# Optimization experiments

Hardware: AMD Instinct MI355X
Metric: run time of the kernel (lower is better)

## Reference

```python
import jax, jax.numpy as jnp
from jax import lax
import numpy as np

T, B, NIN, H, NOUT = 256, 64, 512, 512, 512


def _lstm_dir(x, w_ih, w_hh, b_ih, b_hh, reverse):
    # x: [T,B,NIN]; w_ih: [4H,NIN]; w_hh: [4H,H]
    xg = jnp.einsum('tbi,gi->tbg', x, w_ih) + b_ih + b_hh  # [T,B,4H]
    if reverse:
        xg = xg[::-1]
    h0 = jnp.zeros((x.shape[1], w_hh.shape[1]), x.dtype)

    def step(carry, g):
        h, c = carry
        g = g + h @ w_hh.T
        i, f, gg, o = jnp.split(g, 4, axis=-1)  # PyTorch gate order i,f,g,o
        i = jax.nn.sigmoid(i)
        f = jax.nn.sigmoid(f)
        gg = jnp.tanh(gg)
        o = jax.nn.sigmoid(o)
        c = f * c + i * gg
        h = o * jnp.tanh(c)
        return (h, c), h

    _, hs = lax.scan(step, (h0, h0), xg)
    if reverse:
        hs = hs[::-1]
    return hs  # [T,B,H]


def setup_inputs() -> dict:
    key = jax.random.key(0)
    ks = jax.random.split(key, 12)
    s_in = 1.0 / np.sqrt(H)
    u = lambda k, shape: jax.random.uniform(k, shape, jnp.float32, -s_in, s_in)
    return {
        'x': jax.random.normal(ks[0], (T, B, NIN), jnp.float32),
        'w_ih_f': u(ks[1], (4 * H, NIN)),
        'w_hh_f': u(ks[2], (4 * H, H)),
        'b_ih_f': u(ks[3], (4 * H,)),
        'b_hh_f': u(ks[4], (4 * H,)),
        'w_ih_b': u(ks[5], (4 * H, NIN)),
        'w_hh_b': u(ks[6], (4 * H, H)),
        'b_ih_b': u(ks[7], (4 * H,)),
        'b_hh_b': u(ks[8], (4 * H,)),
        'fc_w': u(ks[9], (NOUT, 2 * H)),
        'fc_b': u(ks[10], (NOUT,)),
    }


def reference(x, w_ih_f, w_hh_f, b_ih_f, b_hh_f, w_ih_b, w_hh_b, b_ih_b, b_hh_b, fc_w, fc_b):
    h_f = _lstm_dir(x, w_ih_f, w_hh_f, b_ih_f, b_hh_f, reverse=False)
    h_b = _lstm_dir(x, w_ih_b, w_hh_b, b_ih_b, b_hh_b, reverse=True)
    h = jnp.concatenate([h_f, h_b], axis=-1)  # [T,B,2H]
    out = jnp.einsum('tbh,oh->tbo', h, fc_w) + fc_b  # fused linear over T*B rows
    return out
```

## Files before the change

kernel.cpp:

```cpp
#include <hip/hip_runtime.h>

typedef unsigned short u16;
typedef unsigned int u32;
typedef unsigned long long u64;
typedef short v8s __attribute__((ext_vector_type(8)));
typedef float v4f __attribute__((ext_vector_type(4)));

#define TT 256
#define BB 64
#define HH 512
#define G4 2048
#define MTB 16384

static __device__ __forceinline__ float bf2f(u16 u) {
    u32 x = ((u32)u) << 16;
    union { u32 i; float f; } c; c.i = x; return c.f;
}
static __device__ __forceinline__ u16 f2bf(float f) {
    union { float f; u32 i; } c; c.f = f;
    u32 u = c.i;
    u += 0x7fffu + ((u >> 16) & 1u);
    return (u16)(u >> 16);
}

__global__ __launch_bounds__(256) void cvt_bf16(const float* __restrict__ src,
                                                u16* __restrict__ dst, int n) {
    int i = blockIdx.x * blockDim.x + threadIdx.x;
    int stride = gridDim.x * blockDim.x;
    for (int j = i * 4; j < n; j += stride * 4) {
        float4 v = *reinterpret_cast<const float4*>(src + j);
        ushort4 o;
        o.x = f2bf(v.x); o.y = f2bf(v.y); o.z = f2bf(v.z); o.w = f2bf(v.w);
        *reinterpret_cast<ushort4*>(dst + j) = o;
    }
}

template<bool OUT_BF16, bool BIAS_M>
__global__ __launch_bounds__(256) void gemm_bt(const u16* __restrict__ A,
                                               const u16* __restrict__ Bm,
                                               void* __restrict__ Cv,
                                               const float* __restrict__ bias1,
                                               const float* __restrict__ bias2,
                                               int M, int N, int K) {
    __shared__ u16 lds_a[128 * 64];
    __shared__ u16 lds_b[128 * 64];
    const int tid = threadIdx.x, lane = tid & 63;
    const int m0 = blockIdx.y * 128, n0 = blockIdx.x * 128;
    const int wid = tid >> 6, wm = wid >> 1, wn = wid & 1;
    v4f acc[4][4] = {};

    const int srow  = tid >> 3;
    const int skoff = (tid & 7) * 8;
    const u16* Ag = A + (size_t)(m0 + srow) * K + skoff;
    const u16* Bg = Bm + (size_t)(n0 + srow) * K + skoff;
    u16* la = lds_a + srow * 64 + skoff;
    u16* lb = lds_b + srow * 64 + skoff;

    for (int k0 = 0; k0 < K; k0 += 64) {
        #pragma unroll
        for (int q = 0; q < 4; ++q) {
            *reinterpret_cast<v8s*>(la + q * 32 * 64) =
                *reinterpret_cast<const v8s*>(Ag + (size_t)q * 32 * K + k0);
            *reinterpret_cast<v8s*>(lb + q * 32 * 64) =
                *reinterpret_cast<const v8s*>(Bg + (size_t)q * 32 * K + k0);
        }
        __syncthreads();
        #pragma unroll
        for (int kk = 0; kk < 2; ++kk) {
            v8s af[4], bfr[4];
            #pragma unroll
            for (int i = 0; i < 4; ++i)
                af[i] = *reinterpret_cast<const v8s*>(
                    lds_a + (wm * 64 + i * 16 + (lane & 15)) * 64 + kk * 32 + (lane >> 4) * 8);
            #pragma unroll
            for (int i = 0; i < 4; ++i)
                bfr[i] = *reinterpret_cast<const v8s*>(
                    lds_b + (wn * 64 + i * 16 + (lane & 15)) * 64 + kk * 32 + (lane >> 4) * 8);
            #pragma unroll
            for (int i = 0; i < 4; ++i)
                #pragma unroll
                for (int j = 0; j < 4; ++j)
                    acc[i][j] = __builtin_amdgcn_mfma_f32_16x16x32_bf16(af[i], bfr[j], acc[i][j], 0, 0, 0);
        }
        __syncthreads();
    }
    #pragma unroll
    for (int i = 0; i < 4; ++i) {
        #pragma unroll
        for (int j = 0; j < 4; ++j) {
            #pragma unroll
            for (int r = 0; r < 4; ++r) {
                int m = m0 + wm * 64 + i * 16 + (lane >> 4) * 4 + r;
                int n = n0 + wn * 64 + j * 16 + (lane & 15);
                float v = acc[i][j][r];
                if (BIAS_M) { v += bias1[m]; if (bias2) v += bias2[m]; }
                else        { v += bias1[n]; }
                if (OUT_BF16) ((u16*)Cv)[(size_t)m * N + n] = f2bf(v);
                else          ((float*)Cv)[(size_t)m * N + n] = v;
            }
        }
    }
}

static __device__ __forceinline__ float sigm(float x) { return 1.f / (1.f + __expf(-x)); }
static __device__ __forceinline__ float tanh_(float x) { return 2.f / (1.f + __expf(-2.f * x)) - 1.f; }

__global__ __launch_bounds__(256, 2) void lstm_persist(
    const u16* __restrict__ w_hh,
    const u16* __restrict__ xgT,
    u16* __restrict__ h_all,
    unsigned* __restrict__ flags)
{
    __shared__ u16 wlds[4 * 16 * 64 * 8];
    const int bx = blockIdx.x;
    const int d = bx >> 5, cg = bx & 31;
    const int lane = threadIdx.x & 63, nf = threadIdx.x >> 6;
    const int lrow = lane & 15, lk = lane >> 4;
    const int b = nf * 16 + lrow;

    {
        const int G = nf;
        const u16* wrow = w_hh + ((size_t)d * G4 + G * HH + cg * 16 + lrow) * HH + lk * 8;
        #pragma unroll
        for (int kk = 0; kk < 16; ++kk)
            *reinterpret_cast<v8s*>(&wlds[((G * 16 + kk) * 64 + lane) * 8]) =
                *reinterpret_cast<const v8s*>(wrow + kk * 32);
    }
    __syncthreads();

    float c[4] = {0.f, 0.f, 0.f, 0.f};
    float xg[4][4];
    unsigned* cnt = flags + (d * 4 + nf) * 64;

    {
        const int t0 = d ? (TT - 1) : 0;
        const u16* xgb = xgT + (size_t)d * G4 * MTB + (size_t)t0 * BB + b;
        #pragma unroll
        for (int G = 0; G < 4; ++G)
            #pragma unroll
            for (int r = 0; r < 4; ++r)
                xg[G][r] = bf2f(xgb[(size_t)(G * HH + cg * 16 + lk * 4 + r) * MTB]);
    }

    for (int s = 0; s < TT; ++s) {
        const int t = d ? (TT - 1 - s) : s;
        v4f acc[4] = {};
        if (s > 0) {
            v8s af0[4][4];
            #pragma unroll
            for (int G = 0; G < 4; ++G)
                #pragma unroll
                for (int kk = 0; kk < 4; ++kk)
                    af0[G][kk] = *reinterpret_cast<const v8s*>(
                        &wlds[((G * 16 + kk) * 64 + lane) * 8]);
            const unsigned tgt = 32u * (unsigned)s;
            while (true) {
                unsigned fv = __hip_atomic_load(cnt, __ATOMIC_RELAXED,
                                                __HIP_MEMORY_SCOPE_AGENT);
                if (__all((int)(fv >= tgt))) break;
            }
            asm volatile("" ::: "memory");
            const int tprev = d ? (t + 1) : (t - 1);
            const u16* hp = h_all + ((size_t)tprev * BB + b) * 1024 + d * HH + lk * 8;
            v8s bf_[16];
            #pragma unroll
            for (int kk = 0; kk < 16; ++kk) {
                union { u64 w[2]; v8s v; } u;
                const u16* p = hp + kk * 32;
                u.w[0] = __hip_atomic_load((const u64*)p,
                                           __ATOMIC_RELAXED, __HIP_MEMORY_SCOPE_AGENT);
                u.w[1] = __hip_atomic_load((const u64*)(p + 4),
                                           __ATOMIC_RELAXED, __HIP_MEMORY_SCOPE_AGENT);
                bf_[kk] = u.v;
            }
            #pragma unroll
            for (int kk = 0; kk < 4; ++kk)
                #pragma unroll
                for (int G = 0; G < 4; ++G)
                    acc[G] = __builtin_amdgcn_mfma_f32_16x16x32_bf16(af0[G][kk], bf_[kk], acc[G], 0, 0, 0);
            #pragma unroll
            for (int kk = 4; kk < 16; ++kk)
                #pragma unroll
                for (int G = 0; G < 4; ++G) {
                    v8s af = *reinterpret_cast<const v8s*>(
                        &wlds[((G * 16 + kk) * 64 + lane) * 8]);
                    acc[G] = __builtin_amdgcn_mfma_f32_16x16x32_bf16(af, bf_[kk], acc[G], 0, 0, 0);
                }
        }
        ushort4 hout;
        #pragma unroll
        for (int r = 0; r < 4; ++r) {
            float pi = acc[0][r] + xg[0][r];
            float pf = acc[1][r] + xg[1][r];
            float pg = acc[2][r] + xg[2][r];
            float po = acc[3][r] + xg[3][r];
            float iv = sigm(pi), fv = sigm(pf), gv = tanh_(pg), ov = sigm(po);
            float cc = fv * c[r] + iv * gv;
            c[r] = cc;
            ((u16*)&hout)[r] = f2bf(ov * tanh_(cc));
        }
        union { ushort4 v; u64 q; } hu; hu.v = hout;
        __hip_atomic_store((u64*)(
                h_all + ((size_t)t * BB + b) * 1024 + d * HH + cg * 16 + lk * 4),
            hu.q, __ATOMIC_RELAXED, __HIP_MEMORY_SCOPE_AGENT);
        asm volatile("s_waitcnt vmcnt(0)" ::: "memory");
        if (lane == 0)
            __hip_atomic_fetch_add(cnt, 1u, __ATOMIC_RELAXED, __HIP_MEMORY_SCOPE_AGENT);
        if (s + 1 < TT) {
            const int tn = d ? (TT - 2 - s) : (s + 1);
            const u16* xgb = xgT + (size_t)d * G4 * MTB + (size_t)tn * BB + b;
            #pragma unroll
            for (int G = 0; G < 4; ++G)
                #pragma unroll
                for (int r = 0; r < 4; ++r)
                    xg[G][r] = bf2f(xgb[(size_t)(G * HH + cg * 16 + lk * 4 + r) * MTB]);
        }
    }
}

extern "C" void kernel_launch(void* const* d_in, const int* in_sizes, int n_in,
                              void* d_out, int out_size, void* d_ws, size_t ws_size,
                              hipStream_t stream) {
    const float* x    = (const float*)d_in[0];
    const float* wihf = (const float*)d_in[1];
    const float* whhf = (const float*)d_in[2];
    const float* bihf = (const float*)d_in[3];
    const float* bhhf = (const float*)d_in[4];
    const float* wihb = (const float*)d_in[5];
    const float* whhb = (const float*)d_in[6];
    const float* bihb = (const float*)d_in[7];
    const float* bhhb = (const float*)d_in[8];
    const float* fcw  = (const float*)d_in[9];
    const float* fcb  = (const float*)d_in[10];

    char* ws = (char*)d_ws;
    size_t off = 0;
    auto alloc = [&](size_t bytes) {
        off = (off + 255) & ~(size_t)255;
        char* p = ws + off; off += bytes; return p;
    };
    u16* x_bf    = (u16*)alloc((size_t)MTB * 512 * 2);
    u16* wih_bf  = (u16*)alloc((size_t)2 * G4 * 512 * 2);
    u16* whh_bf  = (u16*)alloc((size_t)2 * G4 * 512 * 2);
    u16* fcw_bf  = (u16*)alloc((size_t)512 * 1024 * 2);
    u16* xgT     = (u16*)alloc((size_t)2 * G4 * MTB * 2);
    u16* h_all   = (u16*)alloc((size_t)MTB * 1024 * 2);
    unsigned* flags = (unsigned*)alloc(8 * 64 * sizeof(unsigned));
    (void)ws_size;

    cvt_bf16<<<1024, 256, 0, stream>>>(x, x_bf, MTB * 512);
    cvt_bf16<<<256, 256, 0, stream>>>(wihf, wih_bf, G4 * 512);
    cvt_bf16<<<256, 256, 0, stream>>>(wihb, wih_bf + (size_t)G4 * 512, G4 * 512);
    cvt_bf16<<<256, 256, 0, stream>>>(whhf, whh_bf, G4 * 512);
    cvt_bf16<<<256, 256, 0, stream>>>(whhb, whh_bf + (size_t)G4 * 512, G4 * 512);
    cvt_bf16<<<128, 256, 0, stream>>>(fcw, fcw_bf, 512 * 1024);

    gemm_bt<true, true><<<dim3(MTB / 128, G4 / 128), 256, 0, stream>>>(
        wih_bf, x_bf, xgT, bihf, bhhf, G4, MTB, 512);
    gemm_bt<true, true><<<dim3(MTB / 128, G4 / 128), 256, 0, stream>>>(
        wih_bf + (size_t)G4 * 512, x_bf, xgT + (size_t)G4 * MTB, bihb, bhhb, G4, MTB, 512);

    hipMemsetAsync(flags, 0, 8 * 64 * sizeof(unsigned), stream);
    lstm_persist<<<64, 256, 0, stream>>>(whh_bf, xgT, h_all, flags);

    gemm_bt<false, false><<<dim3(512 / 128, MTB / 128), 256, 0, stream>>>(
        h_all, fcw_bf, d_out, fcb, nullptr, MTB, 512, 1024);
}
```

Measured before the change: 1.529 ms.

## Merge LSTM directions per block and replace atomic counters with per-producer flags

```diff
diff --git a/kernel.cpp b/kernel.cpp
--- a/kernel.cpp
+++ b/kernel.cpp
@@ -105,32 +105,34 @@
 static __device__ __forceinline__ float sigm(float x) { return 1.f / (1.f + __expf(-x)); }
 static __device__ __forceinline__ float tanh_(float x) { return 2.f / (1.f + __expf(-2.f * x)) - 1.f; }
 
-__global__ __launch_bounds__(256, 2) void lstm_persist(
+__global__ __launch_bounds__(512, 1) void lstm_persist(
     const u16* __restrict__ w_hh,
     const u16* __restrict__ xgT,
     u16* __restrict__ h_all,
     unsigned* __restrict__ flags)
 {
-    __shared__ u16 wlds[4 * 16 * 64 * 8];
-    const int bx = blockIdx.x;
-    const int d = bx >> 5, cg = bx & 31;
-    const int lane = threadIdx.x & 63, nf = threadIdx.x >> 6;
+    __shared__ u16 wlds[2 * 4 * 16 * 64 * 8];
+    const int cg = blockIdx.x;
+    const int lane = threadIdx.x & 63;
+    const int nf = threadIdx.x >> 6;
+    const int d = nf >> 2, nfb = nf & 3;
     const int lrow = lane & 15, lk = lane >> 4;
-    const int b = nf * 16 + lrow;
+    const int b = nfb * 16 + lrow;
 
     {
-        const int G = nf;
+        const int G = nfb;
         const u16* wrow = w_hh + ((size_t)d * G4 + G * HH + cg * 16 + lrow) * HH + lk * 8;
         #pragma unroll
         for (int kk = 0; kk < 16; ++kk)
-            *reinterpret_cast<v8s*>(&wlds[((G * 16 + kk) * 64 + lane) * 8]) =
+            *reinterpret_cast<v8s*>(&wlds[(((d * 4 + G) * 16 + kk) * 64 + lane) * 8]) =
                 *reinterpret_cast<const v8s*>(wrow + kk * 32);
     }
     __syncthreads();
 
     float c[4] = {0.f, 0.f, 0.f, 0.f};
     float xg[4][4];
-    unsigned* cnt = flags + (d * 4 + nf) * 64;
+    unsigned* fl = flags + (d * 4 + nfb) * 32;
+    const u16* wbase = &wlds[(size_t)d * 4 * 16 * 64 * 8];
 
     {
         const int t0 = d ? (TT - 1) : 0;
@@ -152,12 +154,13 @@
                 #pragma unroll
                 for (int kk = 0; kk < 4; ++kk)
                     af0[G][kk] = *reinterpret_cast<const v8s*>(
-                        &wlds[((G * 16 + kk) * 64 + lane) * 8]);
-            const unsigned tgt = 32u * (unsigned)s;
+                        &wbase[((G * 16 + kk) * 64 + lane) * 8]);
+            const unsigned tgt = (unsigned)s;
             while (true) {
-                unsigned fv = __hip_atomic_load(cnt, __ATOMIC_RELAXED,
-                                                __HIP_MEMORY_SCOPE_AGENT);
+                unsigned fv = __hip_atomic_load(&fl[lane & 31],
+                                                __ATOMIC_RELAXED, __HIP_MEMORY_SCOPE_AGENT);
                 if (__all((int)(fv >= tgt))) break;
+                __builtin_amdgcn_s_sleep(1);
             }
             asm volatile("" ::: "memory");
             const int tprev = d ? (t + 1) : (t - 1);
@@ -183,7 +186,7 @@
                 #pragma unroll
                 for (int G = 0; G < 4; ++G) {
                     v8s af = *reinterpret_cast<const v8s*>(
-                        &wlds[((G * 16 + kk) * 64 + lane) * 8]);
+                        &wbase[((G * 16 + kk) * 64 + lane) * 8]);
                     acc[G] = __builtin_amdgcn_mfma_f32_16x16x32_bf16(af, bf_[kk], acc[G], 0, 0, 0);
                 }
         }
@@ -205,7 +208,8 @@
             hu.q, __ATOMIC_RELAXED, __HIP_MEMORY_SCOPE_AGENT);
         asm volatile("s_waitcnt vmcnt(0)" ::: "memory");
         if (lane == 0)
-            __hip_atomic_fetch_add(cnt, 1u, __ATOMIC_RELAXED, __HIP_MEMORY_SCOPE_AGENT);
+            __hip_atomic_store(&fl[cg], (unsigned)(s + 1),
+                               __ATOMIC_RELAXED, __HIP_MEMORY_SCOPE_AGENT);
         if (s + 1 < TT) {
             const int tn = d ? (TT - 2 - s) : (s + 1);
             const u16* xgb = xgT + (size_t)d * G4 * MTB + (size_t)tn * BB + b;
@@ -245,7 +249,7 @@
     u16* fcw_bf  = (u16*)alloc((size_t)512 * 1024 * 2);
     u16* xgT     = (u16*)alloc((size_t)2 * G4 * MTB * 2);
     u16* h_all   = (u16*)alloc((size_t)MTB * 1024 * 2);
-    unsigned* flags = (unsigned*)alloc(8 * 64 * sizeof(unsigned));
+    unsigned* flags = (unsigned*)alloc(2 * 4 * 32 * sizeof(unsigned));
     (void)ws_size;
 
     cvt_bf16<<<1024, 256, 0, stream>>>(x, x_bf, MTB * 512);
@@ -260,8 +264,8 @@
     gemm_bt<true, true><<<dim3(MTB / 128, G4 / 128), 256, 0, stream>>>(
         wih_bf + (size_t)G4 * 512, x_bf, xgT + (size_t)G4 * MTB, bihb, bhhb, G4, MTB, 512);
 
-    hipMemsetAsync(flags, 0, 8 * 64 * sizeof(unsigned), stream);
-    lstm_persist<<<64, 256, 0, stream>>>(whh_bf, xgT, h_all, flags);
+    hipMemsetAsync(flags, 0, 2 * 4 * 32 * sizeof(unsigned), stream);
+    lstm_persist<<<32, 512, 0, stream>>>(whh_bf, xgT, h_all, flags);
 
     gemm_bt<false, false><<<dim3(512 / 128, MTB / 128), 256, 0, stream>>>(
         h_all, fcw_bf, d_out, fcb, nullptr, MTB, 512, 1024);
```

New measurement: 2.400 ms. 1.57x slower.

## Replace counter-flag sync with timestep-tagged hidden-state ring buffer

Applied to the files above, without the earlier changes.

```diff
diff --git a/kernel.cpp b/kernel.cpp
--- a/kernel.cpp
+++ b/kernel.cpp
@@ -105,11 +105,18 @@
 static __device__ __forceinline__ float sigm(float x) { return 1.f / (1.f + __expf(-x)); }
 static __device__ __forceinline__ float tanh_(float x) { return 2.f / (1.f + __expf(-2.f * x)) - 1.f; }
 
+static __device__ __forceinline__ u64 ald(const u64* p) {
+    return __hip_atomic_load(p, __ATOMIC_RELAXED, __HIP_MEMORY_SCOPE_AGENT);
+}
+static __device__ __forceinline__ u32 packw(u64 q) {
+    return ((u32)q & 0xFFFFu) | ((u32)(q >> 32) << 16);
+}
+
 __global__ __launch_bounds__(256, 2) void lstm_persist(
     const u16* __restrict__ w_hh,
     const u16* __restrict__ xgT,
     u16* __restrict__ h_all,
-    unsigned* __restrict__ flags)
+    u32* __restrict__ ring)
 {
     __shared__ u16 wlds[4 * 16 * 64 * 8];
     const int bx = blockIdx.x;
@@ -130,7 +137,6 @@
 
     float c[4] = {0.f, 0.f, 0.f, 0.f};
     float xg[4][4];
-    unsigned* cnt = flags + (d * 4 + nf) * 64;
 
     {
         const int t0 = d ? (TT - 1) : 0;
@@ -146,47 +152,58 @@
         const int t = d ? (TT - 1 - s) : s;
         v4f acc[4] = {};
         if (s > 0) {
-            v8s af0[4][4];
-            #pragma unroll
-            for (int G = 0; G < 4; ++G)
+            const int tprev = d ? (t + 1) : (t - 1);
+            const u64 expq = (u64)((u32)tprev << 16);
+            const u32* rp = ring + ((size_t)(tprev & 3) * BB + b) * 1024 + d * HH + lk * 8;
+            v8s bf_[16];
+            u32 valid = 0;
+            #pragma unroll
+            for (int kk = 0; kk < 16; ++kk) {
+                const u64* p = (const u64*)(rp + kk * 32);
+                u64 q0 = ald(p), q1 = ald(p + 1), q2 = ald(p + 2), q3 = ald(p + 3);
+                u64 bad = ((q0 ^ expq) | (q1 ^ expq) | (q2 ^ expq) | (q3 ^ expq))
+                          & 0x00000000FFFF0000ULL;
+                union { u32 w[4]; v8s v; } P;
+                P.w[0] = packw(q0); P.w[1] = packw(q1);
+                P.w[2] = packw(q2); P.w[3] = packw(q3);
+                bf_[kk] = P.v;
+                if (__all(bad == 0)) valid |= 1u << kk;
+            }
+            #pragma unroll
+            for (int kk = 0; kk < 16; ++kk)
+                if (valid & (1u << kk)) {
+                    #pragma unroll
+                    for (int G = 0; G < 4; ++G) {
+                        v8s af = *reinterpret_cast<const v8s*>(
+                            &wlds[((G * 16 + kk) * 64 + lane) * 8]);
+                        acc[G] = __builtin_amdgcn_mfma_f32_16x16x32_bf16(af, bf_[kk], acc[G], 0, 0, 0);
+                    }
+                }
+            while (valid != 0xFFFFu) {
                 #pragma unroll
-                for (int kk = 0; kk < 4; ++kk)
-                    af0[G][kk] = *reinterpret_cast<const v8s*>(
-                        &wlds[((G * 16 + kk) * 64 + lane) * 8]);
-            const unsigned tgt = 32u * (unsigned)s;
-            while (true) {
-                unsigned fv = __hip_atomic_load(cnt, __ATOMIC_RELAXED,
-                                                __HIP_MEMORY_SCOPE_AGENT);
-                if (__all((int)(fv >= tgt))) break;
+                for (int kk = 0; kk < 16; ++kk)
+                    if (!(valid & (1u << kk))) {
+                        const u64* p = (const u64*)(rp + kk * 32);
+                        u64 q0 = ald(p), q1 = ald(p + 1), q2 = ald(p + 2), q3 = ald(p + 3);
+                        u64 bad = ((q0 ^ expq) | (q1 ^ expq) | (q2 ^ expq) | (q3 ^ expq))
+                                  & 0x00000000FFFF0000ULL;
+                        if (__all(bad == 0)) {
+                            union { u32 w[4]; v8s v; } P;
+                            P.w[0] = packw(q0); P.w[1] = packw(q1);
+                            P.w[2] = packw(q2); P.w[3] = packw(q3);
+                            #pragma unroll
+                            for (int G = 0; G < 4; ++G) {
+                                v8s af = *reinterpret_cast<const v8s*>(
+                                    &wlds[((G * 16 + kk) * 64 + lane) * 8]);
+                                acc[G] = __builtin_amdgcn_mfma_f32_16x16x32_bf16(af, P.v, acc[G], 0, 0, 0);
+                            }
+                            valid |= 1u << kk;
+                        }
+                    }
             }
-            asm volatile("" ::: "memory");
-            const int tprev = d ? (t + 1) : (t - 1);
-            const u16* hp = h_all + ((size_t)tprev * BB + b) * 1024 + d * HH + lk * 8;
-            v8s bf_[16];
-            #pragma unroll
-            for (int kk = 0; kk < 16; ++kk) {
-                union { u64 w[2]; v8s v; } u;
-                const u16* p = hp + kk * 32;
-                u.w[0] = __hip_atomic_load((const u64*)p,
-                                           __ATOMIC_RELAXED, __HIP_MEMORY_SCOPE_AGENT);
-                u.w[1] = __hip_atomic_load((const u64*)(p + 4),
-                                           __ATOMIC_RELAXED, __HIP_MEMORY_SCOPE_AGENT);
-                bf_[kk] = u.v;
-            }
-            #pragma unroll
-            for (int kk = 0; kk < 4; ++kk)
-                #pragma unroll
-                for (int G = 0; G < 4; ++G)
-                    acc[G] = __builtin_amdgcn_mfma_f32_16x16x32_bf16(af0[G][kk], bf_[kk], acc[G], 0, 0, 0);
-            #pragma unroll
-            for (int kk = 4; kk < 16; ++kk)
-                #pragma unroll
-                for (int G = 0; G < 4; ++G) {
-                    v8s af = *reinterpret_cast<const v8s*>(
-                        &wlds[((G * 16 + kk) * 64 + lane) * 8]);
-                    acc[G] = __builtin_amdgcn_mfma_f32_16x16x32_bf16(af, bf_[kk], acc[G], 0, 0, 0);
-                }
-        }
+        }
+        const u32 tg = (u32)t << 16;
+        u32 hw[4];
         ushort4 hout;
         #pragma unroll
         for (int r = 0; r < 4; ++r) {
@@ -197,15 +214,18 @@
             float iv = sigm(pi), fv = sigm(pf), gv = tanh_(pg), ov = sigm(po);
             float cc = fv * c[r] + iv * gv;
             c[r] = cc;
-            ((u16*)&hout)[r] = f2bf(ov * tanh_(cc));
-        }
+            u16 hv = f2bf(ov * tanh_(cc));
+            hw[r] = tg | (u32)hv;
+            ((u16*)&hout)[r] = hv;
+        }
+        const int j0 = cg * 16 + lk * 4;
+        u64* rq = (u64*)(ring + ((size_t)(t & 3) * BB + b) * 1024 + d * HH + j0);
+        __hip_atomic_store(rq,     (u64)hw[0] | ((u64)hw[1] << 32),
+                           __ATOMIC_RELAXED, __HIP_MEMORY_SCOPE_AGENT);
+        __hip_atomic_store(rq + 1, (u64)hw[2] | ((u64)hw[3] << 32),
+                           __ATOMIC_RELAXED, __HIP_MEMORY_SCOPE_AGENT);
         union { ushort4 v; u64 q; } hu; hu.v = hout;
-        __hip_atomic_store((u64*)(
-                h_all + ((size_t)t * BB + b) * 1024 + d * HH + cg * 16 + lk * 4),
-            hu.q, __ATOMIC_RELAXED, __HIP_MEMORY_SCOPE_AGENT);
-        asm volatile("s_waitcnt vmcnt(0)" ::: "memory");
-        if (lane == 0)
-            __hip_atomic_fetch_add(cnt, 1u, __ATOMIC_RELAXED, __HIP_MEMORY_SCOPE_AGENT);
+        *reinterpret_cast<u64*>(h_all + ((size_t)t * BB + b) * 1024 + d * HH + j0) = hu.q;
         if (s + 1 < TT) {
             const int tn = d ? (TT - 2 - s) : (s + 1);
             const u16* xgb = xgT + (size_t)d * G4 * MTB + (size_t)tn * BB + b;
@@ -245,7 +265,7 @@
     u16* fcw_bf  = (u16*)alloc((size_t)512 * 1024 * 2);
     u16* xgT     = (u16*)alloc((size_t)2 * G4 * MTB * 2);
     u16* h_all   = (u16*)alloc((size_t)MTB * 1024 * 2);
-    unsigned* flags = (unsigned*)alloc(8 * 64 * sizeof(unsigned));
+    u32* ring    = (u32*)alloc((size_t)4 * BB * 1024 * 4);
     (void)ws_size;
 
     cvt_bf16<<<1024, 256, 0, stream>>>(x, x_bf, MTB * 512);
@@ -255,13 +275,14 @@
     cvt_bf16<<<256, 256, 0, stream>>>(whhb, whh_bf + (size_t)G4 * 512, G4 * 512);
     cvt_bf16<<<128, 256, 0, stream>>>(fcw, fcw_bf, 512 * 1024);
 
+    hipMemsetAsync(ring, 0xFF, (size_t)4 * BB * 1024 * 4, stream);
+
     gemm_bt<true, true><<<dim3(MTB / 128, G4 / 128), 256, 0, stream>>>(
         wih_bf, x_bf, xgT, bihf, bhhf, G4, MTB, 512);
     gemm_bt<true, true><<<dim3(MTB / 128, G4 / 128), 256, 0, stream>>>(
         wih_bf + (size_t)G4 * 512, x_bf, xgT + (size_t)G4 * MTB, bihb, bhhb, G4, MTB, 512);
 
-    hipMemsetAsync(flags, 0, 8 * 64 * sizeof(unsigned), stream);
-    lstm_persist<<<64, 256, 0, stream>>>(whh_bf, xgT, h_all, flags);
+    lstm_persist<<<64, 256, 0, stream>>>(whh_bf, xgT, h_all, ring);
 
     gemm_bt<false, false><<<dim3(512 / 128, MTB / 128), 256, 0, stream>>>(
         h_all, fcw_bf, d_out, fcb, nullptr, MTB, 512, 1024);
```

Measured after the change: 3.728 ms. +143.8%, slower.
